# Kernel optimization log

Measured on AMD Instinct MI355X. Metric: run time of the kernel, lower is better.

The kernel has to match this reference:

```python
import jax, jax.numpy as jnp
import numpy as np

N_NODES = 100000


def gcn_conv(x, src, dst, W, b, n_nodes):
    # PyG GCNConv: add self-loops, sym-normalize, transform then aggregate.
    loop = jnp.arange(n_nodes, dtype=src.dtype)
    s = jnp.concatenate([src, loop])
    d = jnp.concatenate([dst, loop])
    ones = jnp.ones(s.shape[0], dtype=x.dtype)
    deg = jax.ops.segment_sum(ones, d, num_segments=n_nodes)
    dinv = jnp.where(deg > 0, jax.lax.rsqrt(deg), 0.0)
    norm = dinv[s] * dinv[d]  # [E+N]
    h = x @ W                 # [N, out]
    msg = h[s] * norm[:, None]
    out = jax.ops.segment_sum(msg, d, num_segments=n_nodes)
    return out + b


def setup_inputs() -> dict:
    key = jax.random.key(0)
    ks = jax.random.split(key, 10)
    n, f = N_NODES, 128
    x = jax.random.normal(ks[0], (n, f), dtype=jnp.float32)
    edge_index = jax.random.randint(ks[1], (2, 1600000), 0, n, dtype=jnp.int64)

    def glorot(k, fin, fout):
        lim = float(np.sqrt(6.0 / (fin + fout)))
        return jax.random.uniform(k, (fin, fout), jnp.float32, -lim, lim)

    return {
        "x": x,
        "edge_index": edge_index,
        "W1": glorot(ks[2], f, 128), "b1": jnp.zeros((128,), jnp.float32),
        "W2": glorot(ks[3], 128, 64), "b2": jnp.zeros((64,), jnp.float32),
        "W3": glorot(ks[4], 64, 32), "b3": jnp.zeros((32,), jnp.float32),
        "Wc": glorot(ks[5], 64, 1), "bc": jnp.zeros((1,), jnp.float32),
    }


def reference(x, edge_index, W1, b1, W2, b2, W3, b3, Wc, bc):
    n = x.shape[0]
    src, dst = edge_index[0], edge_index[1]
    h = jax.nn.relu(gcn_conv(x, src, dst, W1, b1, n))   # dropout: eval mode
    h = jax.nn.relu(gcn_conv(h, src, dst, W2, b2, n))
    h = jax.nn.relu(gcn_conv(h, src, dst, W3, b3, n))
    edge_feat = jnp.concatenate([h[src], h[dst]], axis=1)  # [E, 64]
    return edge_feat @ Wc + bc
```

## Files before the change

kernel.cpp:

```cpp
#include <hip/hip_runtime.h>


typedef unsigned short u16;
typedef short bfrag __attribute__((ext_vector_type(8)));
typedef float ffrag __attribute__((ext_vector_type(4)));

#define BSHIFT 8
#define MAXB   512
#define BIN_CHUNK 4096
#define BCAP   4608

static __device__ __forceinline__ float4 f4add(float4 a, float4 b) {
    return make_float4(a.x + b.x, a.y + b.y, a.z + b.z, a.w + b.w);
}

static __device__ __forceinline__ u16 f2bf(float f) {
    unsigned u = __float_as_uint(f);
    u = (u + 0x7FFFu + ((u >> 16) & 1u)) >> 16;
    return (u16)u;
}

static __device__ __forceinline__ float bflo(unsigned u) {
    return __uint_as_float(u << 16);
}
static __device__ __forceinline__ float bfhi(unsigned u) {
    return __uint_as_float(u & 0xFFFF0000u);
}
static __device__ __forceinline__ void bfacc2(float& a0, float& a1, unsigned u) {
    a0 += bflo(u);
    a1 += bfhi(u);
}
static __device__ __forceinline__ void bfacc8(float* a, uint4 u) {
    bfacc2(a[0], a[1], u.x); bfacc2(a[2], a[3], u.y);
    bfacc2(a[4], a[5], u.z); bfacc2(a[6], a[7], u.w);
}
static __device__ __forceinline__ void bfacc2f(float& a0, float& a1, unsigned u, float v) {
    a0 = fmaf(bflo(u), v, a0);
    a1 = fmaf(bfhi(u), v, a1);
}
static __device__ __forceinline__ void bfacc8f(float* a, uint4 u, float v) {
    bfacc2f(a[0], a[1], u.x, v); bfacc2f(a[2], a[3], u.y, v);
    bfacc2f(a[4], a[5], u.z, v); bfacc2f(a[6], a[7], u.w, v);
}

__global__ __launch_bounds__(256) void prep_w(const float* __restrict__ W1,
                                              u16* __restrict__ w1t,
                                              const float* __restrict__ W2,
                                              u16* __restrict__ w2t) {
    int idx = blockIdx.x * 256 + threadIdx.x;
    if (idx < 128 * 128) {
        int n = idx >> 7, k = idx & 127;
        w1t[idx] = f2bf(W1[k * 128 + n]);
    } else if (idx < 128 * 128 + 64 * 128) {
        int j = idx - 128 * 128;
        int n = j >> 7, k = j & 127;
        w2t[j] = f2bf(W2[k * 64 + n]);
    }
}

__global__ __launch_bounds__(256, 2)
void k_front(const u16* __restrict__ w1t,
             const int* __restrict__ src, const int* __restrict__ dst,
             int* __restrict__ bcur0, unsigned* __restrict__ pairs,
             const float* __restrict__ x, u16* __restrict__ G,
             int E, int B, int N, int BINB) {
    __shared__ __align__(16) u16 xs[64 * 128];
    const int t = threadIdx.x;
    int bid = blockIdx.x;

    if (bid < BINB) {
        int* h    = reinterpret_cast<int*>(xs);
        int* base = h + MAXB;
        const int e0 = bid * BIN_CHUNK;
        const int eEnd = min(e0 + BIN_CHUNK, E);
        for (int i = t; i < B; i += 256) h[i] = 0;
        __syncthreads();
        for (int e = e0 + t; e < eEnd; e += 256)
            atomicAdd(&h[dst[e] >> BSHIFT], 1);
        __syncthreads();
        for (int i = t; i < B; i += 256) {
            int c = h[i];
            base[i] = c ? atomicAdd(&bcur0[i], c) : 0;
            h[i] = 0;
        }
        __syncthreads();
        for (int e = e0 + t; e < eEnd; e += 256) {
            int d = dst[e];
            int b = d >> BSHIFT;
            int pos = b * BCAP + base[b] + atomicAdd(&h[b], 1);
            pairs[pos] = ((unsigned)(d & 255) << 24) | (unsigned)src[e];
        }
        return;
    }
    bid -= BINB;

    const int wave = t >> 6;
    const int lane = t & 63;
    const int l15 = lane & 15;
    const int quad = lane >> 4;
    const int r0 = bid * 64;

    bfrag Bf[8][4];
    #pragma unroll
    for (int nt = 0; nt < 8; nt++)
        #pragma unroll
        for (int kk = 0; kk < 4; kk++)
            Bf[nt][kk] = *reinterpret_cast<const bfrag*>(
                &w1t[(size_t)(nt * 16 + l15) * 128 + kk * 32 + quad * 8]);

    #pragma unroll
    for (int i = 0; i < 4; i++) {
        int v = t + 256 * i;
        int row = v >> 4;
        int cb = v & 15;
        uint4 pack = make_uint4(0, 0, 0, 0);
        if (r0 + row < N) {
            const float4* p = reinterpret_cast<const float4*>(
                &x[(size_t)(r0 + row) * 128 + cb * 8]);
            float4 lo = p[0], hi = p[1];
            pack.x = f2bf(lo.x) | ((unsigned)f2bf(lo.y) << 16);
            pack.y = f2bf(lo.z) | ((unsigned)f2bf(lo.w) << 16);
            pack.z = f2bf(hi.x) | ((unsigned)f2bf(hi.y) << 16);
            pack.w = f2bf(hi.z) | ((unsigned)f2bf(hi.w) << 16);
        }
        int cbs = cb ^ (row & 7);
        *reinterpret_cast<uint4*>(&xs[row * 128 + cbs * 8]) = pack;
    }
    __syncthreads();

    ffrag acc[8];
    #pragma unroll
    for (int nt = 0; nt < 8; nt++) {
        acc[nt][0] = 0.f; acc[nt][1] = 0.f; acc[nt][2] = 0.f; acc[nt][3] = 0.f;
    }

    const int arow = wave * 16 + l15;
    #pragma unroll
    for (int kk = 0; kk < 4; kk++) {
        int cb = (kk * 4 + quad) ^ (l15 & 7);
        bfrag a = *reinterpret_cast<const bfrag*>(&xs[arow * 128 + cb * 8]);
        #pragma unroll
        for (int nt = 0; nt < 8; nt++)
            acc[nt] = __builtin_amdgcn_mfma_f32_16x16x32_bf16(a, Bf[nt][kk], acc[nt], 0, 0, 0);
    }

    #pragma unroll
    for (int nt = 0; nt < 8; nt++)
        #pragma unroll
        for (int r = 0; r < 4; r++) {
            int rl = wave * 16 + quad * 4 + r;
            int grow = r0 + rl;
            if (grow < N)
                G[(size_t)grow * 128 + nt * 16 + l15] = f2bf(acc[nt][r]);
        }
}

__global__ __launch_bounds__(256) void build_csr(const unsigned* __restrict__ pairs,
                                                 const int* __restrict__ bcur0,
                                                 int* __restrict__ rowp,
                                                 int* __restrict__ rowe,
                                                 float* __restrict__ dinv,
                                                 int* __restrict__ ssrc, int N) {
    __shared__ int s[256];
    __shared__ int cur[256];
    const int t = threadIdx.x;
    const int b = blockIdx.x;
    const int eBeg = b * BCAP, eEnd = b * BCAP + bcur0[b];
    const int nodeBase = b << BSHIFT;
    s[t] = 0;
    __syncthreads();
    for (int e = eBeg + t; e < eEnd; e += 256)
        atomicAdd(&s[pairs[e] >> 24], 1);
    __syncthreads();
    const int v = s[t];
    #pragma unroll
    for (int off = 1; off < 256; off <<= 1) {
        int add = (t >= off) ? s[t - off] : 0;
        __syncthreads();
        s[t] += add;
        __syncthreads();
    }
    const int rp = eBeg + s[t] - v;
    const int node = nodeBase + t;
    if (node < N) {
        rowp[node] = rp;
        rowe[node] = rp + v;
        dinv[node] = rsqrtf((float)(v + 1));
    }
    cur[t] = rp;
    __syncthreads();
    for (int e = eBeg + t; e < eEnd; e += 256) {
        unsigned p = pairs[e];
        int pos = atomicAdd(&cur[p >> 24], 1);
        ssrc[pos] = (int)(p & 0xFFFFFFu);
    }
}

__global__ __launch_bounds__(256) void agg1_gemm2(const u16* __restrict__ G,
                                                  const int* __restrict__ rowp,
                                                  const int* __restrict__ rowe,
                                                  const int* __restrict__ ssrc,
                                                  const float* __restrict__ dinv,
                                                  const float* __restrict__ bias,
                                                  const u16* __restrict__ w2t,
                                                  u16* __restrict__ g2, int N) {
    __shared__ __align__(16) u16 hl[16][136];
    __shared__ float ldv[16];
    const int t = threadIdx.x;
    const int wave = t >> 6;
    const int lane = t & 63;
    const int l15 = lane & 15;
    const int quad = lane >> 4;
    const int lj = t & 15;
    const int dn = t >> 4;
    const int d0 = blockIdx.x * 16;
    const int d = d0 + dn;

    if (t < 16) ldv[t] = (d0 + t < N) ? dinv[d0 + t] : 0.f;

    uint4 pk = make_uint4(0, 0, 0, 0);
    if (d < N) {
        const uint4* G4 = reinterpret_cast<const uint4*>(G);
        const float dvd = dinv[d];
        float a[8];
        #pragma unroll
        for (int i = 0; i < 8; i++) a[i] = 0.f;
        bfacc8f(a, G4[(size_t)d * 16 + lj], dvd);
        int e = rowp[d];
        const int end = rowe[d];
        for (; e + 8 <= end; e += 8) {
            int s0 = ssrc[e],     s1 = ssrc[e + 1], s2 = ssrc[e + 2], s3 = ssrc[e + 3];
            int s4 = ssrc[e + 4], s5 = ssrc[e + 5], s6 = ssrc[e + 6], s7 = ssrc[e + 7];
            float v0 = dinv[s0], v1 = dinv[s1], v2 = dinv[s2], v3 = dinv[s3];
            float v4 = dinv[s4], v5 = dinv[s5], v6 = dinv[s6], v7 = dinv[s7];
            uint4 u0 = G4[(size_t)s0 * 16 + lj];
            uint4 u1 = G4[(size_t)s1 * 16 + lj];
            uint4 u2 = G4[(size_t)s2 * 16 + lj];
            uint4 u3 = G4[(size_t)s3 * 16 + lj];
            uint4 u4 = G4[(size_t)s4 * 16 + lj];
            uint4 u5 = G4[(size_t)s5 * 16 + lj];
            uint4 u6 = G4[(size_t)s6 * 16 + lj];
            uint4 u7 = G4[(size_t)s7 * 16 + lj];
            bfacc8f(a, u0, v0); bfacc8f(a, u1, v1); bfacc8f(a, u2, v2); bfacc8f(a, u3, v3);
            bfacc8f(a, u4, v4); bfacc8f(a, u5, v5); bfacc8f(a, u6, v6); bfacc8f(a, u7, v7);
        }
        for (; e + 4 <= end; e += 4) {
            int s0 = ssrc[e], s1 = ssrc[e + 1], s2 = ssrc[e + 2], s3 = ssrc[e + 3];
            float v0 = dinv[s0], v1 = dinv[s1], v2 = dinv[s2], v3 = dinv[s3];
            uint4 u0 = G4[(size_t)s0 * 16 + lj];
            uint4 u1 = G4[(size_t)s1 * 16 + lj];
            uint4 u2 = G4[(size_t)s2 * 16 + lj];
            uint4 u3 = G4[(size_t)s3 * 16 + lj];
            bfacc8f(a, u0, v0); bfacc8f(a, u1, v1); bfacc8f(a, u2, v2); bfacc8f(a, u3, v3);
        }
        for (; e < end; e++) {
            int s = ssrc[e];
            bfacc8f(a, G4[(size_t)s * 16 + lj], dinv[s]);
        }
        const float4 b0 = reinterpret_cast<const float4*>(bias)[lj * 2];
        const float4 b1 = reinterpret_cast<const float4*>(bias)[lj * 2 + 1];
        float h[8];
        h[0] = fmaxf(a[0] * dvd + b0.x, 0.f);
        h[1] = fmaxf(a[1] * dvd + b0.y, 0.f);
        h[2] = fmaxf(a[2] * dvd + b0.z, 0.f);
        h[3] = fmaxf(a[3] * dvd + b0.w, 0.f);
        h[4] = fmaxf(a[4] * dvd + b1.x, 0.f);
        h[5] = fmaxf(a[5] * dvd + b1.y, 0.f);
        h[6] = fmaxf(a[6] * dvd + b1.z, 0.f);
        h[7] = fmaxf(a[7] * dvd + b1.w, 0.f);
        pk.x = f2bf(h[0]) | ((unsigned)f2bf(h[1]) << 16);
        pk.y = f2bf(h[2]) | ((unsigned)f2bf(h[3]) << 16);
        pk.z = f2bf(h[4]) | ((unsigned)f2bf(h[5]) << 16);
        pk.w = f2bf(h[6]) | ((unsigned)f2bf(h[7]) << 16);
    }
    *reinterpret_cast<uint4*>(&hl[dn][lj * 8]) = pk;
    __syncthreads();

    bfrag Bf[4];
    #pragma unroll
    for (int kk = 0; kk < 4; kk++)
        Bf[kk] = *reinterpret_cast<const bfrag*>(
            &w2t[(size_t)(wave * 16 + l15) * 128 + kk * 32 + quad * 8]);

    ffrag acc;
    acc[0] = 0.f; acc[1] = 0.f; acc[2] = 0.f; acc[3] = 0.f;
    #pragma unroll
    for (int kk = 0; kk < 4; kk++) {
        bfrag av = *reinterpret_cast<const bfrag*>(&hl[l15][kk * 32 + quad * 8]);
        acc = __builtin_amdgcn_mfma_f32_16x16x32_bf16(av, Bf[kk], acc, 0, 0, 0);
    }
    #pragma unroll
    for (int r = 0; r < 4; r++) {
        int row = quad * 4 + r;
        int node = d0 + row;
        if (node < N)
            g2[(size_t)node * 64 + wave * 16 + l15] = f2bf(acc[r] * ldv[row]);
    }
}

__global__ __launch_bounds__(256) void agg2_gemm3(const u16* __restrict__ G,
                                                  const int* __restrict__ rowp,
                                                  const int* __restrict__ rowe,
                                                  const int* __restrict__ ssrc,
                                                  const float* __restrict__ dinv,
                                                  const float* __restrict__ bias,
                                                  const float* __restrict__ W3,
                                                  float* __restrict__ g3, int N) {
    __shared__ __align__(16) float wl[64 * 32];
    __shared__ __align__(16) float hl[32][68];
    const int t = threadIdx.x;
    {
        const float4* s4 = reinterpret_cast<const float4*>(W3);
        float4* d4 = reinterpret_cast<float4*>(wl);
        d4[t] = s4[t];
        d4[t + 256] = s4[t + 256];
    }
    __syncthreads();
    const int lj = t & 7;
    const int dn = t >> 3;
    const int d = blockIdx.x * 32 + dn;
    if (d >= N) return;

    const uint4* G4 = reinterpret_cast<const uint4*>(G);
    float a[8];
    #pragma unroll
    for (int i = 0; i < 8; i++) a[i] = 0.f;
    bfacc8(a, G4[(size_t)d * 8 + lj]);
    int e = rowp[d];
    const int end = rowe[d];
    for (; e + 8 <= end; e += 8) {
        int s0 = ssrc[e],     s1 = ssrc[e + 1], s2 = ssrc[e + 2], s3 = ssrc[e + 3];
        int s4 = ssrc[e + 4], s5 = ssrc[e + 5], s6 = ssrc[e + 6], s7 = ssrc[e + 7];
        uint4 u0 = G4[(size_t)s0 * 8 + lj];
        uint4 u1 = G4[(size_t)s1 * 8 + lj];
        uint4 u2 = G4[(size_t)s2 * 8 + lj];
        uint4 u3 = G4[(size_t)s3 * 8 + lj];
        uint4 u4 = G4[(size_t)s4 * 8 + lj];
        uint4 u5 = G4[(size_t)s5 * 8 + lj];
        uint4 u6 = G4[(size_t)s6 * 8 + lj];
        uint4 u7 = G4[(size_t)s7 * 8 + lj];
        bfacc8(a, u0); bfacc8(a, u1); bfacc8(a, u2); bfacc8(a, u3);
        bfacc8(a, u4); bfacc8(a, u5); bfacc8(a, u6); bfacc8(a, u7);
    }
    for (; e + 4 <= end; e += 4) {
        int s0 = ssrc[e], s1 = ssrc[e + 1], s2 = ssrc[e + 2], s3 = ssrc[e + 3];
        uint4 u0 = G4[(size_t)s0 * 8 + lj];
        uint4 u1 = G4[(size_t)s1 * 8 + lj];
        uint4 u2 = G4[(size_t)s2 * 8 + lj];
        uint4 u3 = G4[(size_t)s3 * 8 + lj];
        bfacc8(a, u0); bfacc8(a, u1); bfacc8(a, u2); bfacc8(a, u3);
    }
    for (; e < end; e++)
        bfacc8(a, G4[(size_t)ssrc[e] * 8 + lj]);
    const float dv = dinv[d];
    const float4 b0 = reinterpret_cast<const float4*>(bias)[lj * 2];
    const float4 b1 = reinterpret_cast<const float4*>(bias)[lj * 2 + 1];
    float h[8];
    h[0] = fmaxf(a[0] * dv + b0.x, 0.f);
    h[1] = fmaxf(a[1] * dv + b0.y, 0.f);
    h[2] = fmaxf(a[2] * dv + b0.z, 0.f);
    h[3] = fmaxf(a[3] * dv + b0.w, 0.f);
    h[4] = fmaxf(a[4] * dv + b1.x, 0.f);
    h[5] = fmaxf(a[5] * dv + b1.y, 0.f);
    h[6] = fmaxf(a[6] * dv + b1.z, 0.f);
    h[7] = fmaxf(a[7] * dv + b1.w, 0.f);
    *reinterpret_cast<float4*>(&hl[dn][lj * 8])     = make_float4(h[0], h[1], h[2], h[3]);
    *reinterpret_cast<float4*>(&hl[dn][lj * 8 + 4]) = make_float4(h[4], h[5], h[6], h[7]);
    float g[4] = {0.f, 0.f, 0.f, 0.f};
    #pragma unroll 4
    for (int k4 = 0; k4 < 16; k4++) {
        float4 hv = *reinterpret_cast<const float4*>(&hl[dn][k4 * 4]);
        float hs[4] = {hv.x, hv.y, hv.z, hv.w};
        #pragma unroll
        for (int p = 0; p < 4; p++) {
            float4 w = *reinterpret_cast<const float4*>(&wl[(k4 * 4 + p) * 32 + lj * 4]);
            g[0] += hs[p] * w.x; g[1] += hs[p] * w.y;
            g[2] += hs[p] * w.z; g[3] += hs[p] * w.w;
        }
    }
    *reinterpret_cast<float4*>(&g3[(size_t)d * 32 + lj * 4]) =
        make_float4(g[0] * dv, g[1] * dv, g[2] * dv, g[3] * dv);
}

__global__ __launch_bounds__(256) void aggregate_l3s(const float* __restrict__ G,
                                                     const int* __restrict__ rowp,
                                                     const int* __restrict__ rowe,
                                                     const int* __restrict__ ssrc,
                                                     const float* __restrict__ dinv,
                                                     const float* __restrict__ bias,
                                                     const float* __restrict__ Wc,
                                                     float2* __restrict__ ab, int N) {
    constexpr int L = 8;
    const int t = threadIdx.x;
    const int lj = t % L;
    const int d = blockIdx.x * 32 + t / L;
    if (d >= N) return;

    const float4* G4 = reinterpret_cast<const float4*>(G);
    float4 acc = G4[(size_t)d * L + lj];
    int e = rowp[d];
    const int end = rowe[d];
    for (; e + 8 <= end; e += 8) {
        int s0 = ssrc[e],     s1 = ssrc[e + 1], s2 = ssrc[e + 2], s3 = ssrc[e + 3];
        int s4 = ssrc[e + 4], s5 = ssrc[e + 5], s6 = ssrc[e + 6], s7 = ssrc[e + 7];
        float4 v0 = G4[(size_t)s0 * L + lj];
        float4 v1 = G4[(size_t)s1 * L + lj];
        float4 v2 = G4[(size_t)s2 * L + lj];
        float4 v3 = G4[(size_t)s3 * L + lj];
        float4 v4 = G4[(size_t)s4 * L + lj];
        float4 v5 = G4[(size_t)s5 * L + lj];
        float4 v6 = G4[(size_t)s6 * L + lj];
        float4 v7 = G4[(size_t)s7 * L + lj];
        acc = f4add(acc, f4add(f4add(f4add(v0, v1), f4add(v2, v3)),
                               f4add(f4add(v4, v5), f4add(v6, v7))));
    }
    for (; e + 4 <= end; e += 4) {
        int s0 = ssrc[e], s1 = ssrc[e + 1], s2 = ssrc[e + 2], s3 = ssrc[e + 3];
        float4 v0 = G4[(size_t)s0 * L + lj];
        float4 v1 = G4[(size_t)s1 * L + lj];
        float4 v2 = G4[(size_t)s2 * L + lj];
        float4 v3 = G4[(size_t)s3 * L + lj];
        acc = f4add(acc, f4add(f4add(v0, v1), f4add(v2, v3)));
    }
    for (; e < end; e++)
        acc = f4add(acc, G4[(size_t)ssrc[e] * L + lj]);
    const float dv = dinv[d];
    const float4 b4 = reinterpret_cast<const float4*>(bias)[lj];
    float4 h;
    h.x = fmaxf(acc.x * dv + b4.x, 0.f);
    h.y = fmaxf(acc.y * dv + b4.y, 0.f);
    h.z = fmaxf(acc.z * dv + b4.z, 0.f);
    h.w = fmaxf(acc.w * dv + b4.w, 0.f);
    const float4 wa = reinterpret_cast<const float4*>(Wc)[lj];
    const float4 wb = reinterpret_cast<const float4*>(Wc + 32)[lj];
    float p = h.x * wa.x + h.y * wa.y + h.z * wa.z + h.w * wa.w;
    float q = h.x * wb.x + h.y * wb.y + h.z * wb.z + h.w * wb.w;
    p += __shfl_xor(p, 1); q += __shfl_xor(q, 1);
    p += __shfl_xor(p, 2); q += __shfl_xor(q, 2);
    p += __shfl_xor(p, 4); q += __shfl_xor(q, 4);
    if (lj == 0) ab[d] = make_float2(p, q);
}


__global__ __launch_bounds__(256) void edge_out(const int* __restrict__ src,
                                                const int* __restrict__ dst,
                                                const float2* __restrict__ ab,
                                                const float* __restrict__ bc,
                                                float* __restrict__ out, int E) {
    int e = blockIdx.x * 256 + threadIdx.x;
    if (e < E) out[e] = ab[src[e]].x + ab[dst[e]].y + bc[0];
}

extern "C" void kernel_launch(void* const* d_in, const int* in_sizes, int n_in,
                              void* d_out, int out_size, void* d_ws, size_t ws_size,
                              hipStream_t stream) {
    const float* x  = (const float*)d_in[0];
    const int*   ei = (const int*)d_in[1];
    const float* W1 = (const float*)d_in[2];
    const float* b1 = (const float*)d_in[3];
    const float* W2 = (const float*)d_in[4];
    const float* b2 = (const float*)d_in[5];
    const float* W3 = (const float*)d_in[6];
    const float* b3 = (const float*)d_in[7];
    const float* Wc = (const float*)d_in[8];
    const float* bc = (const float*)d_in[9];
    float* out = (float*)d_out;

    const int N = in_sizes[0] / 128;
    const int E = in_sizes[1] / 2;
    const int B = (N + 255) >> BSHIFT;
    const int* src = ei;
    const int* dst = ei + E;

    size_t off = 0;
    auto alloc = [&](size_t bytes) -> void* {
        size_t o = (off + 255) & ~(size_t)255;
        off = o + bytes;
        return (void*)((char*)d_ws + o);
    };
    float* dinv = (float*)alloc((size_t)N * 4);
    int*   rowp = (int*)alloc((size_t)N * 4);
    int*   rowe = (int*)alloc((size_t)N * 4);
    int*   bcur = (int*)alloc((size_t)(B + 1) * 4);
    int*   ssrc = (int*)alloc((size_t)B * BCAP * 4);
    u16*   w1t  = (u16*)alloc(128 * 128 * 2);
    u16*   w2t  = (u16*)alloc(64 * 128 * 2);
    u16*   g16  = (u16*)alloc((size_t)N * 128 * 2);
    u16*   g2b  = (u16*)alloc((size_t)N * 64 * 2);
    float2* ab  = (float2*)alloc((size_t)N * 8);
    (void)ws_size; (void)n_in; (void)out_size;

    unsigned* pairs = (unsigned*)g2b;
    float* g3f = (float*)g16;

    const int gE = (E + 255) / 256;
    const int gR = (N + 63) / 64;
    const int BINB = (E + BIN_CHUNK - 1) / BIN_CHUNK;

    hipMemsetAsync(bcur, 0, (size_t)(B + 1) * 4, stream);

    prep_w<<<96, 256, 0, stream>>>(W1, w1t, W2, w2t);
    k_front<<<BINB + gR, 256, 0, stream>>>(w1t, src, dst, bcur, pairs, x, g16,
                                           E, B, N, BINB);
    build_csr<<<B, 256, 0, stream>>>(pairs, bcur, rowp, rowe, dinv, ssrc, N);

    agg1_gemm2<<<(N + 15) / 16, 256, 0, stream>>>(g16, rowp, rowe, ssrc, dinv, b1, w2t, g2b, N);
    agg2_gemm3<<<(N + 31) / 32, 256, 0, stream>>>(g2b, rowp, rowe, ssrc, dinv, b2, W3, g3f, N);
    aggregate_l3s<<<(N + 31) / 32, 256, 0, stream>>>(g3f, rowp, rowe, ssrc, dinv, b3, Wc, ab, N);

    edge_out<<<gE, 256, 0, stream>>>(src, dst, ab, bc, out, E);
}
```

Before: 316.8 us.

## Regroup front kernels: merge weight prep with binning, CSR build with GEMM1

The launch sequence changes from prep_w, then binning fused with the layer-1 GEMM, then CSR build, to two kernels. The first does weight conversion alongside edge binning, and the second does CSR build alongside the layer-1 GEMM. This removes one kernel launch and overlaps CSR construction with the MFMA GEMM instead of overlapping binning with it. It also drops the 8-wide unrolled gather loop in layer-1 aggregation, leaving the 4-wide loop, which may reduce register pressure but exposes fewer loads in flight.

Result: no change. 311.1 us (-1.8%).

```diff
diff --git a/kernel.cpp b/kernel.cpp
--- a/kernel.cpp
+++ b/kernel.cpp
@@ -43,56 +43,100 @@
     bfacc2f(a[4], a[5], u.z, v); bfacc2f(a[6], a[7], u.w, v);
 }
 
-__global__ __launch_bounds__(256) void prep_w(const float* __restrict__ W1,
-                                              u16* __restrict__ w1t,
-                                              const float* __restrict__ W2,
-                                              u16* __restrict__ w2t) {
-    int idx = blockIdx.x * 256 + threadIdx.x;
-    if (idx < 128 * 128) {
-        int n = idx >> 7, k = idx & 127;
-        w1t[idx] = f2bf(W1[k * 128 + n]);
-    } else if (idx < 128 * 128 + 64 * 128) {
-        int j = idx - 128 * 128;
-        int n = j >> 7, k = j & 127;
-        w2t[j] = f2bf(W2[k * 64 + n]);
+__global__ __launch_bounds__(256) void k_prepbin(const float* __restrict__ W1,
+                                                 u16* __restrict__ w1t,
+                                                 const float* __restrict__ W2,
+                                                 u16* __restrict__ w2t,
+                                                 const int* __restrict__ src,
+                                                 const int* __restrict__ dst,
+                                                 int* __restrict__ bcur0,
+                                                 unsigned* __restrict__ pairs,
+                                                 int E, int B, int BINB) {
+    __shared__ int h[MAXB];
+    __shared__ int base[MAXB];
+    const int t = threadIdx.x;
+    int bid = blockIdx.x;
+    if (bid < 96) {
+        int idx = bid * 256 + t;
+        if (idx < 128 * 128) {
+            int n = idx >> 7, k = idx & 127;
+            w1t[idx] = f2bf(W1[k * 128 + n]);
+        } else if (idx < 128 * 128 + 64 * 128) {
+            int j = idx - 128 * 128;
+            int n = j >> 7, k = j & 127;
+            w2t[j] = f2bf(W2[k * 64 + n]);
+        }
+        return;
+    }
+    bid -= 96;
+    if (bid >= BINB) return;
+    const int e0 = bid * BIN_CHUNK;
+    const int eEnd = min(e0 + BIN_CHUNK, E);
+    for (int i = t; i < B; i += 256) h[i] = 0;
+    __syncthreads();
+    for (int e = e0 + t; e < eEnd; e += 256)
+        atomicAdd(&h[dst[e] >> BSHIFT], 1);
+    __syncthreads();
+    for (int i = t; i < B; i += 256) {
+        int c = h[i];
+        base[i] = c ? atomicAdd(&bcur0[i], c) : 0;
+        h[i] = 0;
+    }
+    __syncthreads();
+    for (int e = e0 + t; e < eEnd; e += 256) {
+        int d = dst[e];
+        int b = d >> BSHIFT;
+        int pos = b * BCAP + base[b] + atomicAdd(&h[b], 1);
+        pairs[pos] = ((unsigned)(d & 255) << 24) | (unsigned)src[e];
     }
 }
 
 __global__ __launch_bounds__(256, 2)
-void k_front(const u16* __restrict__ w1t,
-             const int* __restrict__ src, const int* __restrict__ dst,
-             int* __restrict__ bcur0, unsigned* __restrict__ pairs,
-             const float* __restrict__ x, u16* __restrict__ G,
-             int E, int B, int N, int BINB) {
+void k_mid(const unsigned* __restrict__ pairs, const int* __restrict__ bcur0,
+           int* __restrict__ rowp, int* __restrict__ rowe,
+           float* __restrict__ dinv, int* __restrict__ ssrc,
+           const u16* __restrict__ w1t, const float* __restrict__ x,
+           u16* __restrict__ G, int N, int B) {
     __shared__ __align__(16) u16 xs[64 * 128];
     const int t = threadIdx.x;
     int bid = blockIdx.x;
 
-    if (bid < BINB) {
-        int* h    = reinterpret_cast<int*>(xs);
-        int* base = h + MAXB;
-        const int e0 = bid * BIN_CHUNK;
-        const int eEnd = min(e0 + BIN_CHUNK, E);
-        for (int i = t; i < B; i += 256) h[i] = 0;
+    if (bid < B) {
+        int* s   = reinterpret_cast<int*>(xs);
+        int* cur = s + 256;
+        const int b = bid;
+        const int eBeg = b * BCAP, eEnd = b * BCAP + bcur0[b];
+        const int nodeBase = b << BSHIFT;
+        s[t] = 0;
         __syncthreads();
-        for (int e = e0 + t; e < eEnd; e += 256)
-            atomicAdd(&h[dst[e] >> BSHIFT], 1);
+        for (int e = eBeg + t; e < eEnd; e += 256)
+            atomicAdd(&s[pairs[e] >> 24], 1);
         __syncthreads();
-        for (int i = t; i < B; i += 256) {
-            int c = h[i];
-            base[i] = c ? atomicAdd(&bcur0[i], c) : 0;
-            h[i] = 0;
-        }
+        const int v = s[t];
+        #pragma unroll
+        for (int off = 1; off < 256; off <<= 1) {
+            int add = (t >= off) ? s[t - off] : 0;
+            __syncthreads();
+            s[t] += add;
+            __syncthreads();
+        }
+        const int rp = eBeg + s[t] - v;
+        const int node = nodeBase + t;
+        if (node < N) {
+            rowp[node] = rp;
+            rowe[node] = rp + v;
+            dinv[node] = rsqrtf((float)(v + 1));
+        }
+        cur[t] = rp;
         __syncthreads();
-        for (int e = e0 + t; e < eEnd; e += 256) {
-            int d = dst[e];
-            int b = d >> BSHIFT;
-            int pos = b * BCAP + base[b] + atomicAdd(&h[b], 1);
-            pairs[pos] = ((unsigned)(d & 255) << 24) | (unsigned)src[e];
+        for (int e = eBeg + t; e < eEnd; e += 256) {
+            unsigned p = pairs[e];
+            int pos = atomicAdd(&cur[p >> 24], 1);
+            ssrc[pos] = (int)(p & 0xFFFFFFu);
         }
         return;
     }
-    bid -= BINB;
+    bid -= B;
 
     const int wave = t >> 6;
     const int lane = t & 63;
@@ -153,47 +197,6 @@
             if (grow < N)
                 G[(size_t)grow * 128 + nt * 16 + l15] = f2bf(acc[nt][r]);
         }
-}
-
-__global__ __launch_bounds__(256) void build_csr(const unsigned* __restrict__ pairs,
-                                                 const int* __restrict__ bcur0,
-                                                 int* __restrict__ rowp,
-                                                 int* __restrict__ rowe,
-                                                 float* __restrict__ dinv,
-                                                 int* __restrict__ ssrc, int N) {
-    __shared__ int s[256];
-    __shared__ int cur[256];
-    const int t = threadIdx.x;
-    const int b = blockIdx.x;
-    const int eBeg = b * BCAP, eEnd = b * BCAP + bcur0[b];
-    const int nodeBase = b << BSHIFT;
-    s[t] = 0;
-    __syncthreads();
-    for (int e = eBeg + t; e < eEnd; e += 256)
-        atomicAdd(&s[pairs[e] >> 24], 1);
-    __syncthreads();
-    const int v = s[t];
-    #pragma unroll
-    for (int off = 1; off < 256; off <<= 1) {
-        int add = (t >= off) ? s[t - off] : 0;
-        __syncthreads();
-        s[t] += add;
-        __syncthreads();
-    }
-    const int rp = eBeg + s[t] - v;
-    const int node = nodeBase + t;
-    if (node < N) {
-        rowp[node] = rp;
-        rowe[node] = rp + v;
-        dinv[node] = rsqrtf((float)(v + 1));
-    }
-    cur[t] = rp;
-    __syncthreads();
-    for (int e = eBeg + t; e < eEnd; e += 256) {
-        unsigned p = pairs[e];
-        int pos = atomicAdd(&cur[p >> 24], 1);
-        ssrc[pos] = (int)(p & 0xFFFFFFu);
-    }
 }
 
 __global__ __launch_bounds__(256) void agg1_gemm2(const u16* __restrict__ G,
@@ -228,22 +231,6 @@
         bfacc8f(a, G4[(size_t)d * 16 + lj], dvd);
         int e = rowp[d];
         const int end = rowe[d];
-        for (; e + 8 <= end; e += 8) {
-            int s0 = ssrc[e],     s1 = ssrc[e + 1], s2 = ssrc[e + 2], s3 = ssrc[e + 3];
-            int s4 = ssrc[e + 4], s5 = ssrc[e + 5], s6 = ssrc[e + 6], s7 = ssrc[e + 7];
-            float v0 = dinv[s0], v1 = dinv[s1], v2 = dinv[s2], v3 = dinv[s3];
-            float v4 = dinv[s4], v5 = dinv[s5], v6 = dinv[s6], v7 = dinv[s7];
-            uint4 u0 = G4[(size_t)s0 * 16 + lj];
-            uint4 u1 = G4[(size_t)s1 * 16 + lj];
-            uint4 u2 = G4[(size_t)s2 * 16 + lj];
-            uint4 u3 = G4[(size_t)s3 * 16 + lj];
-            uint4 u4 = G4[(size_t)s4 * 16 + lj];
-            uint4 u5 = G4[(size_t)s5 * 16 + lj];
-            uint4 u6 = G4[(size_t)s6 * 16 + lj];
-            uint4 u7 = G4[(size_t)s7 * 16 + lj];
-            bfacc8f(a, u0, v0); bfacc8f(a, u1, v1); bfacc8f(a, u2, v2); bfacc8f(a, u3, v3);
-            bfacc8f(a, u4, v4); bfacc8f(a, u5, v5); bfacc8f(a, u6, v6); bfacc8f(a, u7, v7);
-        }
         for (; e + 4 <= end; e += 4) {
             int s0 = ssrc[e], s1 = ssrc[e + 1], s2 = ssrc[e + 2], s3 = ssrc[e + 3];
             float v0 = dinv[s0], v1 = dinv[s1], v2 = dinv[s2], v3 = dinv[s3];
@@ -499,10 +486,10 @@
 
     hipMemsetAsync(bcur, 0, (size_t)(B + 1) * 4, stream);
 
-    prep_w<<<96, 256, 0, stream>>>(W1, w1t, W2, w2t);
-    k_front<<<BINB + gR, 256, 0, stream>>>(w1t, src, dst, bcur, pairs, x, g16,
-                                           E, B, N, BINB);
-    build_csr<<<B, 256, 0, stream>>>(pairs, bcur, rowp, rowe, dinv, ssrc, N);
+    k_prepbin<<<96 + BINB, 256, 0, stream>>>(W1, w1t, W2, w2t, src, dst, bcur,
+                                             pairs, E, B, BINB);
+    k_mid<<<B + gR, 256, 0, stream>>>(pairs, bcur, rowp, rowe, dinv, ssrc,
+                                      w1t, x, g16, N, B);
 
     agg1_gemm2<<<(N + 15) / 16, 256, 0, stream>>>(g16, rowp, rowe, ssrc, dinv, b1, w2t, g2b, N);
     agg2_gemm3<<<(N + 31) / 32, 256, 0, stream>>>(g2b, rowp, rowe, ssrc, dinv, b2, W3, g3f, N);
```
